# Kernel optimization log

Measured on AMD Instinct MI355X. Metric: run time of the kernel, lower is better.

The kernel has to match this reference:

```python
import jax, jax.numpy as jnp
import numpy as np

N_NODES = 100000
N_EDGES = 3200000
IN_CH = 128
HID = 128
N_CLASSES = 32
N_GRAPHS = 256


def gcn_conv(x, W, b, src, dst, n_nodes):
    """PyG GCNConv: add self-loops, symmetric deg^-1/2 normalization,
    linear transform, gather-scatter aggregation, bias."""
    xw = x @ W  # [N, out]
    loop = jnp.arange(n_nodes, dtype=src.dtype)
    s = jnp.concatenate([src, loop])  # sources incl. self-loops
    d = jnp.concatenate([dst, loop])  # targets incl. self-loops
    deg = jax.ops.segment_sum(jnp.ones_like(d, dtype=xw.dtype), d,
                              num_segments=n_nodes)
    dinv = jnp.where(deg > 0, jax.lax.rsqrt(deg), 0.0)
    norm = dinv[s] * dinv[d]  # [E+N]
    msgs = xw[s] * norm[:, None]  # gather + scale
    out = jax.ops.segment_sum(msgs, d, num_segments=n_nodes)  # scatter-add
    return out + b


def global_mean_pool(x, batch, n_graphs):
    sums = jax.ops.segment_sum(x, batch, num_segments=n_graphs)
    cnt = jax.ops.segment_sum(jnp.ones((x.shape[0],), x.dtype), batch,
                              num_segments=n_graphs)
    return sums / jnp.maximum(cnt, 1.0)[:, None]


def setup_inputs() -> dict:
    key = jax.random.key(0)
    ks = jax.random.split(key, 9)
    x = jax.random.normal(ks[0], (N_NODES, IN_CH), dtype=jnp.float32)
    edge_index = jax.random.randint(ks[1], (2, N_EDGES), 0, N_NODES, dtype=jnp.int32)
    batch = jnp.sort(jax.random.randint(ks[2], (N_NODES,), 0, N_GRAPHS, dtype=jnp.int32))
    s1 = 1.0 / np.sqrt(IN_CH)
    s2 = 1.0 / np.sqrt(HID)
    W1 = jax.random.uniform(ks[3], (IN_CH, HID), jnp.float32, -s1, s1)
    b1 = jnp.zeros((HID,), jnp.float32)
    W2 = jax.random.uniform(ks[4], (HID, HID), jnp.float32, -s2, s2)
    b2 = jnp.zeros((HID,), jnp.float32)
    Wfc = jax.random.uniform(ks[5], (HID, N_CLASSES), jnp.float32, -s2, s2)
    bfc = jax.random.uniform(ks[6], (N_CLASSES,), jnp.float32, -s2, s2)
    return {"x": x, "edge_index": edge_index, "batch": batch,
            "W1": W1, "b1": b1, "W2": W2, "b2": b2, "Wfc": Wfc, "bfc": bfc}


def reference(x, edge_index, batch, W1, b1, W2, b2, Wfc, bfc):
    src, dst = edge_index[0], edge_index[1]
    h = jax.nn.relu(gcn_conv(x, W1, b1, src, dst, N_NODES))
    h = jax.nn.relu(gcn_conv(h, W2, b2, src, dst, N_NODES))
    g = global_mean_pool(h, batch, N_GRAPHS)  # [G, HID]
    return g @ Wfc + bfc  # [G, N_CLASSES]
```

## Files before the change

### kernel.cpp

```cpp
#include <hip/hip_runtime.h>
#include <hip/hip_bf16.h>
#include <hip/hip_fp16.h>

static constexpr int CH     = 128;
static constexpr int NCLS   = 32;
static constexpr int NGRAPH = 256;

static constexpr int BSHIFT = 8;
static constexpr int BW     = 1 << BSHIFT;
static constexpr int MAXB   = 512;

typedef _Float16 half8 __attribute__((ext_vector_type(8)));
typedef _Float16 half4 __attribute__((ext_vector_type(4)));
typedef float    f32x4 __attribute__((ext_vector_type(4)));
typedef float    f32x2 __attribute__((ext_vector_type(2)));

static constexpr float FP8_SCALE = 64.0f;
static constexpr float FP8_INV   = 1.0f / 64.0f;

__device__ __forceinline__ f32x2 dec8(unsigned short u) {
  return __builtin_amdgcn_cvt_pk_f32_fp8((int)u, false);
}
__device__ __forceinline__ unsigned char enc8(float v) {
  return (unsigned char)(__builtin_amdgcn_cvt_pk_fp8_f32(v, v, 0, false) & 0xFF);
}

__global__ __launch_bounds__(256) void k_init_wt(
    int* __restrict__ gcur, int CAP, int NBUCK, int* __restrict__ xzero,
    const float* __restrict__ W1, const float* __restrict__ W2,
    _Float16* __restrict__ WhT1, _Float16* __restrict__ WhT2) {
  int t = threadIdx.x;
  if (blockIdx.x == 0) {
    for (int i = t; i < NBUCK; i += 256) gcur[i] = i * CAP;
    if (t < 32) xzero[t] = 0;
    return;
  }
  int i = (blockIdx.x - 1) * 256 + t;
  const float* W = (i < CH * CH) ? W1 : W2;
  _Float16* T   = (i < CH * CH) ? WhT1 : WhT2;
  int j = i & (CH * CH - 1);
  int k = j >> 7, n = j & 127;
  T[n * CH + k] = (_Float16)W[j];
}

__global__ __launch_bounds__(1024) void k_scatter(
    const int* __restrict__ src, const int* __restrict__ dst,
    int* __restrict__ gcur, int* __restrict__ ebuf, int E) {
  __shared__ int bcnt[MAXB];
  __shared__ int bbase[MAXB];
  int t = threadIdx.x;
  if (t < MAXB) bcnt[t] = 0;
  __syncthreads();
  int base = blockIdx.x * 8192;
  int s_[8], d_[8], r_[8];
  #pragma unroll
  for (int j = 0; j < 8; ++j) {
    int i = base + j * 1024 + t;
    if (i < E) {
      s_[j] = src[i];
      d_[j] = dst[i];
      r_[j] = atomicAdd(&bcnt[d_[j] >> BSHIFT], 1);
    }
  }
  __syncthreads();
  if (t < MAXB && bcnt[t]) bbase[t] = atomicAdd(&gcur[t], bcnt[t]);
  __syncthreads();
  #pragma unroll
  for (int j = 0; j < 8; ++j) {
    int i = base + j * 1024 + t;
    if (i < E) {
      int b = d_[j] >> BSHIFT;
      int p = ((d_[j] & (BW - 1)) << 17) | s_[j];
      ebuf[bbase[b] + r_[j]] = p;
    }
  }
}

__global__ __launch_bounds__(1024) void k_build(
    const int* __restrict__ ebuf, const int* __restrict__ gcur,
    int* __restrict__ offs, int* __restrict__ oend,
    float* __restrict__ dinv, int* __restrict__ csr, int N, int CAP) {
  __shared__ int sdeg[BW];
  __shared__ int sscan[BW];
  int b = blockIdx.x;
  int t = threadIdx.x;
  int lo = b << BSHIFT;
  int e0 = b * CAP;
  int e1 = gcur[b];

  if (t < BW) sdeg[t] = 0;
  __syncthreads();
  for (int e = e0 + t; e < e1; e += 1024)
    atomicAdd(&sdeg[ebuf[e] >> 17], 1);
  __syncthreads();
  if (t < BW) sscan[t] = (sdeg[t] + 3) & ~3;
  __syncthreads();
  for (int st = 1; st < BW; st <<= 1) {
    int v = (t < BW && t >= st) ? sscan[t - st] : 0;
    __syncthreads();
    if (t < BW) sscan[t] += v;
    __syncthreads();
  }
  if (t < BW) {
    int deg  = sdeg[t];
    int pdeg = (deg + 3) & ~3;
    int ex = b * CAP + sscan[t] - pdeg;
    int n = lo + t;
    if (n < N) {
      offs[n] = ex;
      oend[n] = ex + deg;
      dinv[n] = 1.0f / sqrtf((float)(deg + 1));
      for (int q = deg; q < pdeg; ++q) csr[ex + q] = N;
    }
    sscan[t] = ex;
  }
  __syncthreads();
  for (int e = e0 + t; e < e1; e += 1024) {
    int p = ebuf[e];
    int pos = atomicAdd(&sscan[p >> 17], 1);
    csr[pos] = p & 0x1FFFF;
  }
}

__device__ __forceinline__ void stage_w(const _Float16* __restrict__ WhT,
                                        _Float16 (*Ws)[136], int tid) {
  #pragma unroll
  for (int l = 0; l < 8; ++l) {
    int idx = tid + l * 256;
    int n = idx >> 4, k8 = (idx & 15) << 3;
    *(half8*)&Ws[n][k8] = *(const half8*)(WhT + n * CH + k8);
  }
}

__device__ __forceinline__ void gemm_core64(
    const _Float16 (*As)[136], const _Float16 (*Ws)[136],
    const float* __restrict__ dinv, unsigned char* __restrict__ C,
    int row0, int M, int tid) {
  int lane = tid & 63, wave = tid >> 6;
  int quad = lane >> 4, sub = lane & 15;
  int m0 = wave * 16;

  f32x4 acc[8];
  #pragma unroll
  for (int j = 0; j < 8; ++j) acc[j] = (f32x4){0.f, 0.f, 0.f, 0.f};

  #pragma unroll
  for (int kc = 0; kc < 4; ++kc) {
    int ko = kc * 32 + quad * 8;
    half8 a = *(const half8*)&As[m0 + sub][ko];
    #pragma unroll
    for (int nt = 0; nt < 8; ++nt) {
      half8 b = *(const half8*)&Ws[nt * 16 + sub][ko];
      acc[nt] = __builtin_amdgcn_mfma_f32_16x16x32_f16(a, b, acc[nt], 0, 0, 0);
    }
  }
  #pragma unroll
  for (int r = 0; r < 4; ++r) {
    int row = row0 + m0 + quad * 4 + r;
    if (row < M) {
      float d = dinv[row] * FP8_SCALE;
      #pragma unroll
      for (int nt = 0; nt < 8; ++nt)
        C[(size_t)row * CH + nt * 16 + sub] = enc8(acc[nt][r] * d);
    }
  }
}

__global__ __launch_bounds__(256) void k_gemm_f32(
    const float* __restrict__ A, const _Float16* __restrict__ WhT,
    const float* __restrict__ dinv, unsigned char* __restrict__ C, int M) {
  __shared__ _Float16 As[64][136];
  __shared__ _Float16 Ws[128][136];
  int tid = threadIdx.x;
  int row0 = blockIdx.x * 64;
  #pragma unroll
  for (int l = 0; l < 8; ++l) {
    int idx = tid + l * 256;
    int r = idx >> 5, c4 = (idx & 31) << 2;
    int rr = row0 + r; if (rr >= M) rr = M - 1;
    float4 v = *(const float4*)(A + (size_t)rr * CH + c4);
    half4 hv = { (_Float16)v.x, (_Float16)v.y, (_Float16)v.z, (_Float16)v.w };
    *(half4*)&As[r][c4] = hv;
  }
  stage_w(WhT, Ws, tid);
  __syncthreads();
  gemm_core64(As, Ws, dinv, C, row0, M, tid);
}

__global__ __launch_bounds__(256) void k_gemm_f16(
    const _Float16* __restrict__ A, const _Float16* __restrict__ WhT,
    const float* __restrict__ dinv, unsigned char* __restrict__ C, int M) {
  __shared__ _Float16 As[64][136];
  __shared__ _Float16 Ws[128][136];
  int tid = threadIdx.x;
  int row0 = blockIdx.x * 64;
  #pragma unroll
  for (int l = 0; l < 4; ++l) {
    int idx = tid + l * 256;
    int r = idx >> 4, c8 = (idx & 15) << 3;
    int rr = row0 + r; if (rr >= M) rr = M - 1;
    *(half8*)&As[r][c8] = *(const half8*)(A + (size_t)rr * CH + c8);
  }
  stage_w(WhT, Ws, tid);
  __syncthreads();
  gemm_core64(As, Ws, dinv, C, row0, M, tid);
}

__global__ __launch_bounds__(256) void k_agg(
    const unsigned char* __restrict__ xs, const int* __restrict__ csr,
    const int* __restrict__ offs, const int* __restrict__ oend,
    const float* __restrict__ dinv, const float* __restrict__ bias,
    __half* __restrict__ out, int N) {
  int wid  = blockIdx.x * 4 + (threadIdx.x >> 6);
  int lane = threadIdx.x & 63;
  int nA = wid * 2, nB = nA + 1;
  if (nA >= N) return;
  bool hasB = (nB < N);
  unsigned int lane2 = (unsigned int)lane << 1;

  int eA = offs[nA];
  int cA = (oend[nA] - eA + 3) >> 2;
  int eB = hasB ? offs[nB] : 0;
  int cB = hasB ? ((oend[nB] - eB + 3) >> 2) : 0;

  f32x2 aA0 = dec8(*(const unsigned short*)(xs + (((unsigned int)nA << 7) | lane2)));
  f32x2 aA1 = {0.f, 0.f};
  f32x2 aB0 = {0.f, 0.f}, aB1 = {0.f, 0.f};
  if (hasB)
    aB0 = dec8(*(const unsigned short*)(xs + (((unsigned int)nB << 7) | lane2)));

  while (cA > 0 && cB > 0) {
    int4 ca = *(const int4*)(csr + eA);
    int4 cb = *(const int4*)(csr + eB);
    unsigned short uA0 = *(const unsigned short*)(xs + (((unsigned int)ca.x << 7) | lane2));
    unsigned short uA1 = *(const unsigned short*)(xs + (((unsigned int)ca.y << 7) | lane2));
    unsigned short uA2 = *(const unsigned short*)(xs + (((unsigned int)ca.z << 7) | lane2));
    unsigned short uA3 = *(const unsigned short*)(xs + (((unsigned int)ca.w << 7) | lane2));
    unsigned short uB0 = *(const unsigned short*)(xs + (((unsigned int)cb.x << 7) | lane2));
    unsigned short uB1 = *(const unsigned short*)(xs + (((unsigned int)cb.y << 7) | lane2));
    unsigned short uB2 = *(const unsigned short*)(xs + (((unsigned int)cb.z << 7) | lane2));
    unsigned short uB3 = *(const unsigned short*)(xs + (((unsigned int)cb.w << 7) | lane2));
    aA0 += dec8(uA0); aA1 += dec8(uA1); aA0 += dec8(uA2); aA1 += dec8(uA3);
    aB0 += dec8(uB0); aB1 += dec8(uB1); aB0 += dec8(uB2); aB1 += dec8(uB3);
    eA += 4; eB += 4; --cA; --cB;
  }
  while (cA > 0) {
    int4 ca = *(const int4*)(csr + eA);
    unsigned short u0 = *(const unsigned short*)(xs + (((unsigned int)ca.x << 7) | lane2));
    unsigned short u1 = *(const unsigned short*)(xs + (((unsigned int)ca.y << 7) | lane2));
    unsigned short u2 = *(const unsigned short*)(xs + (((unsigned int)ca.z << 7) | lane2));
    unsigned short u3 = *(const unsigned short*)(xs + (((unsigned int)ca.w << 7) | lane2));
    aA0 += dec8(u0); aA1 += dec8(u1); aA0 += dec8(u2); aA1 += dec8(u3);
    eA += 4; --cA;
  }
  while (cB > 0) {
    int4 cb = *(const int4*)(csr + eB);
    unsigned short u0 = *(const unsigned short*)(xs + (((unsigned int)cb.x << 7) | lane2));
    unsigned short u1 = *(const unsigned short*)(xs + (((unsigned int)cb.y << 7) | lane2));
    unsigned short u2 = *(const unsigned short*)(xs + (((unsigned int)cb.z << 7) | lane2));
    unsigned short u3 = *(const unsigned short*)(xs + (((unsigned int)cb.w << 7) | lane2));
    aB0 += dec8(u0); aB1 += dec8(u1); aB0 += dec8(u2); aB1 += dec8(u3);
    eB += 4; --cB;
  }

  float2 bxy = *(const float2*)(bias + 2 * lane);
  {
    f32x2 s = aA0 + aA1;
    float dn = dinv[nA] * FP8_INV;
    float rx = fmaf(s[0], dn, bxy.x);
    float ry = fmaf(s[1], dn, bxy.y);
    ((__half2*)out)[(size_t)nA * 64 + lane] =
        __floats2half2_rn(fmaxf(rx, 0.f), fmaxf(ry, 0.f));
  }
  if (hasB) {
    f32x2 s = aB0 + aB1;
    float dn = dinv[nB] * FP8_INV;
    float rx = fmaf(s[0], dn, bxy.x);
    float ry = fmaf(s[1], dn, bxy.y);
    ((__half2*)out)[(size_t)nB * 64 + lane] =
        __floats2half2_rn(fmaxf(rx, 0.f), fmaxf(ry, 0.f));
  }
}

__global__ __launch_bounds__(128) void k_pool(
    const __half* __restrict__ h, const int* __restrict__ batch,
    float* __restrict__ gsum, int* __restrict__ gstart,
    int* __restrict__ gend, int N) {
  int ch = threadIdx.x;
  int n0 = blockIdx.x * 128;
  int n1 = n0 + 128; if (n1 > N) n1 = N;
  if (n0 >= N) return;
  for (int n = n0 + ch; n < n1; n += 128) {
    int g = batch[n];
    if (n == 0 || batch[n - 1] != g) gstart[g] = n;
    if (n == N - 1 || batch[n + 1] != g) gend[g] = n + 1;
  }
  float acc = 0.f;
  int curg = batch[n0];
  for (int n = n0; n < n1; ++n) {
    int g = batch[n];
    if (g != curg) {
      atomicAdd(&gsum[curg * CH + ch], acc);
      acc = 0.f; curg = g;
    }
    acc += __half2float(h[(size_t)n * CH + ch]);
  }
  atomicAdd(&gsum[curg * CH + ch], acc);
}

__global__ __launch_bounds__(64) void k_fc(
    const float* __restrict__ gsum, const int* __restrict__ gstart,
    const int* __restrict__ gend, const float* __restrict__ Wfc,
    const float* __restrict__ bfc, float* __restrict__ outp) {
  int g = blockIdx.x;
  int j = threadIdx.x;
  if (j >= NCLS) return;
  int cnt = gend[g] - gstart[g];
  float invc = 1.0f / fmaxf((float)cnt, 1.0f);
  float acc = 0.0f;
  for (int c = 0; c < CH; ++c)
    acc = fmaf(gsum[g * CH + c], Wfc[c * NCLS + j], acc);
  outp[g * NCLS + j] = fmaf(acc, invc, bfc[j]);
}

extern "C" void kernel_launch(void* const* d_in, const int* in_sizes, int n_in,
                              void* d_out, int out_size, void* d_ws, size_t ws_size,
                              hipStream_t stream) {
  const float* x    = (const float*)d_in[0];
  const int*   ei   = (const int*)d_in[1];
  const int*   batch= (const int*)d_in[2];
  const float* W1   = (const float*)d_in[3];
  const float* b1   = (const float*)d_in[4];
  const float* W2   = (const float*)d_in[5];
  const float* b2   = (const float*)d_in[6];
  const float* Wfc  = (const float*)d_in[7];
  const float* bfc  = (const float*)d_in[8];
  float* outp = (float*)d_out;

  const int N = in_sizes[0] / CH;
  const int E = in_sizes[1] / 2;
  const int* src = ei;
  const int* dst = ei + E;
  const int NBUCK = (N + BW - 1) >> BSHIFT;
  int CAP = (E / NBUCK) + (E / NBUCK) / 8 + 1280;
  CAP = (CAP + 3) & ~3;

  char* w = (char*)d_ws;
  size_t o = 0;
  auto carve = [&](size_t bytes) -> void* {
    o = (o + 255) & ~(size_t)255;
    void* p = w + o;
    o += bytes;
    return p;
  };
  float*    gsum   = (float*)   carve((size_t)NGRAPH * CH * 4);
  int*      gstart = (int*)     carve((size_t)NGRAPH * 4);
  int*      gend   = (int*)     carve((size_t)NGRAPH * 4);
  size_t zbytes = o;
  int*      offs   = (int*)     carve((size_t)N * 4);
  int*      oendb  = (int*)     carve((size_t)N * 4);
  int*      gcur   = (int*)     carve(MAXB * 4);
  int*      csr    = (int*)     carve((size_t)NBUCK * CAP * 4);
  float*    dinv   = (float*)   carve((size_t)N * 4);
  _Float16* WhT1   = (_Float16*)carve((size_t)CH * CH * 2);
  _Float16* WhT2   = (_Float16*)carve((size_t)CH * CH * 2);
  unsigned char* xsbuf = (unsigned char*)carve((size_t)(N + 1) * CH);
  __half*   hbuf   = (__half*)  carve((size_t)N * CH * 2);
  (void)ws_size;

  int* ebuf = (int*)hbuf;

  (void)hipMemsetAsync(gsum, 0, zbytes, stream);

  const int GB64 = (N + 63) / 64;
  const int GB   = (N + 127) / 128;
  const int AB   = (N + 7) / 8;

  k_init_wt<<<129, 256, 0, stream>>>(gcur, CAP, NBUCK,
                                     (int*)(xsbuf + (size_t)N * CH),
                                     W1, W2, WhT1, WhT2);
  k_scatter<<<(E + 8191) / 8192, 1024, 0, stream>>>(src, dst, gcur, ebuf, E);
  k_build  <<<NBUCK, 1024, 0, stream>>>(ebuf, gcur, offs, oendb, dinv, csr, N, CAP);

  k_gemm_f32<<<GB64, 256, 0, stream>>>(x, WhT1, dinv, xsbuf, N);
  k_agg<<<AB, 256, 0, stream>>>(xsbuf, csr, offs, oendb, dinv, b1, hbuf, N);
  k_gemm_f16<<<GB64, 256, 0, stream>>>((const _Float16*)hbuf, WhT2, dinv, xsbuf, N);
  k_agg<<<AB, 256, 0, stream>>>(xsbuf, csr, offs, oendb, dinv, b2, hbuf, N);

  k_pool<<<GB, 128, 0, stream>>>(hbuf, batch, gsum, gstart, gend, N);
  k_fc<<<NGRAPH, 64, 0, stream>>>(gsum, gstart, gend, Wfc, bfc, outp);
  (void)out_size; (void)n_in;
}
```

Before: 360.5 us.

## Use persistent grid-stride aggregation with 8-wide unrolled gathers and prefetched indices

The aggregation kernel becomes a persistent grid-stride loop capped at 2048 blocks, where each wave processes node pairs repeatedly instead of launching one wave per pair. The inner loop now issues 16 gathers per iteration, 8 edges per node, and prefetches the next CSR index quads while the current gathers are in flight, to raise memory-level parallelism. Tails are drained in 8- and 4-edge chunks. The cost is higher register pressure and possible load imbalance across the fixed grid. It also reads CSR entries one iteration ahead, which depends on padding after each segment.

```diff
diff --git a/kernel.cpp b/kernel.cpp
--- a/kernel.cpp
+++ b/kernel.cpp
@@ -211,74 +211,88 @@
     const int* __restrict__ offs, const int* __restrict__ oend,
     const float* __restrict__ dinv, const float* __restrict__ bias,
     __half* __restrict__ out, int N) {
-  int wid  = blockIdx.x * 4 + (threadIdx.x >> 6);
-  int lane = threadIdx.x & 63;
-  int nA = wid * 2, nB = nA + 1;
-  if (nA >= N) return;
-  bool hasB = (nB < N);
+  int wid0  = blockIdx.x * 4 + (threadIdx.x >> 6);
+  int lane  = threadIdx.x & 63;
+  int wstep = gridDim.x * 4;
   unsigned int lane2 = (unsigned int)lane << 1;
-
-  int eA = offs[nA];
-  int cA = (oend[nA] - eA + 3) >> 2;
-  int eB = hasB ? offs[nB] : 0;
-  int cB = hasB ? ((oend[nB] - eB + 3) >> 2) : 0;
-
-  f32x2 aA0 = dec8(*(const unsigned short*)(xs + (((unsigned int)nA << 7) | lane2)));
-  f32x2 aA1 = {0.f, 0.f};
-  f32x2 aB0 = {0.f, 0.f}, aB1 = {0.f, 0.f};
-  if (hasB)
-    aB0 = dec8(*(const unsigned short*)(xs + (((unsigned int)nB << 7) | lane2)));
-
-  while (cA > 0 && cB > 0) {
-    int4 ca = *(const int4*)(csr + eA);
-    int4 cb = *(const int4*)(csr + eB);
-    unsigned short uA0 = *(const unsigned short*)(xs + (((unsigned int)ca.x << 7) | lane2));
-    unsigned short uA1 = *(const unsigned short*)(xs + (((unsigned int)ca.y << 7) | lane2));
-    unsigned short uA2 = *(const unsigned short*)(xs + (((unsigned int)ca.z << 7) | lane2));
-    unsigned short uA3 = *(const unsigned short*)(xs + (((unsigned int)ca.w << 7) | lane2));
-    unsigned short uB0 = *(const unsigned short*)(xs + (((unsigned int)cb.x << 7) | lane2));
-    unsigned short uB1 = *(const unsigned short*)(xs + (((unsigned int)cb.y << 7) | lane2));
-    unsigned short uB2 = *(const unsigned short*)(xs + (((unsigned int)cb.z << 7) | lane2));
-    unsigned short uB3 = *(const unsigned short*)(xs + (((unsigned int)cb.w << 7) | lane2));
-    aA0 += dec8(uA0); aA1 += dec8(uA1); aA0 += dec8(uA2); aA1 += dec8(uA3);
-    aB0 += dec8(uB0); aB1 += dec8(uB1); aB0 += dec8(uB2); aB1 += dec8(uB3);
-    eA += 4; eB += 4; --cA; --cB;
-  }
-  while (cA > 0) {
-    int4 ca = *(const int4*)(csr + eA);
-    unsigned short u0 = *(const unsigned short*)(xs + (((unsigned int)ca.x << 7) | lane2));
-    unsigned short u1 = *(const unsigned short*)(xs + (((unsigned int)ca.y << 7) | lane2));
-    unsigned short u2 = *(const unsigned short*)(xs + (((unsigned int)ca.z << 7) | lane2));
-    unsigned short u3 = *(const unsigned short*)(xs + (((unsigned int)ca.w << 7) | lane2));
-    aA0 += dec8(u0); aA1 += dec8(u1); aA0 += dec8(u2); aA1 += dec8(u3);
-    eA += 4; --cA;
-  }
-  while (cB > 0) {
-    int4 cb = *(const int4*)(csr + eB);
-    unsigned short u0 = *(const unsigned short*)(xs + (((unsigned int)cb.x << 7) | lane2));
-    unsigned short u1 = *(const unsigned short*)(xs + (((unsigned int)cb.y << 7) | lane2));
-    unsigned short u2 = *(const unsigned short*)(xs + (((unsigned int)cb.z << 7) | lane2));
-    unsigned short u3 = *(const unsigned short*)(xs + (((unsigned int)cb.w << 7) | lane2));
-    aB0 += dec8(u0); aB1 += dec8(u1); aB0 += dec8(u2); aB1 += dec8(u3);
-    eB += 4; --cB;
-  }
-
   float2 bxy = *(const float2*)(bias + 2 * lane);
-  {
-    f32x2 s = aA0 + aA1;
-    float dn = dinv[nA] * FP8_INV;
-    float rx = fmaf(s[0], dn, bxy.x);
-    float ry = fmaf(s[1], dn, bxy.y);
-    ((__half2*)out)[(size_t)nA * 64 + lane] =
-        __floats2half2_rn(fmaxf(rx, 0.f), fmaxf(ry, 0.f));
-  }
-  if (hasB) {
-    f32x2 s = aB0 + aB1;
-    float dn = dinv[nB] * FP8_INV;
-    float rx = fmaf(s[0], dn, bxy.x);
-    float ry = fmaf(s[1], dn, bxy.y);
-    ((__half2*)out)[(size_t)nB * 64 + lane] =
-        __floats2half2_rn(fmaxf(rx, 0.f), fmaxf(ry, 0.f));
+
+  auto g = [&](int s) -> unsigned short {
+    return *(const unsigned short*)(xs + (((unsigned int)s << 7) | lane2));
+  };
+
+  for (int wid = wid0; wid * 2 < N; wid += wstep) {
+    int nA = wid * 2, nB = nA + 1;
+    bool hasB = (nB < N);
+
+    int eA = offs[nA];
+    int cA = (oend[nA] - eA + 3) >> 2;
+    int eB = hasB ? offs[nB] : eA;
+    int cB = hasB ? ((oend[nB] - eB + 3) >> 2) : 0;
+
+    f32x2 aA0 = dec8(g(nA));
+    f32x2 aA1 = {0.f, 0.f};
+    f32x2 aB0 = {0.f, 0.f}, aB1 = {0.f, 0.f};
+    if (hasB) aB0 = dec8(g(nB));
+
+    if (cA >= 2 && cB >= 2) {
+      int4 ca0 = *(const int4*)(csr + eA);
+      int4 ca1 = *(const int4*)(csr + eA + 4);
+      int4 cb0 = *(const int4*)(csr + eB);
+      int4 cb1 = *(const int4*)(csr + eB + 4);
+      do {
+        unsigned short uA0 = g(ca0.x), uA1 = g(ca0.y), uA2 = g(ca0.z), uA3 = g(ca0.w);
+        unsigned short uA4 = g(ca1.x), uA5 = g(ca1.y), uA6 = g(ca1.z), uA7 = g(ca1.w);
+        unsigned short uB0 = g(cb0.x), uB1 = g(cb0.y), uB2 = g(cb0.z), uB3 = g(cb0.w);
+        unsigned short uB4 = g(cb1.x), uB5 = g(cb1.y), uB6 = g(cb1.z), uB7 = g(cb1.w);
+        eA += 8; eB += 8; cA -= 2; cB -= 2;
+        int4 na0 = *(const int4*)(csr + eA);
+        int4 na1 = *(const int4*)(csr + eA + 4);
+        int4 nb0 = *(const int4*)(csr + eB);
+        int4 nb1 = *(const int4*)(csr + eB + 4);
+        aA0 += dec8(uA0); aA1 += dec8(uA1); aA0 += dec8(uA2); aA1 += dec8(uA3);
+        aA0 += dec8(uA4); aA1 += dec8(uA5); aA0 += dec8(uA6); aA1 += dec8(uA7);
+        aB0 += dec8(uB0); aB1 += dec8(uB1); aB0 += dec8(uB2); aB1 += dec8(uB3);
+        aB0 += dec8(uB4); aB1 += dec8(uB5); aB0 += dec8(uB6); aB1 += dec8(uB7);
+        ca0 = na0; ca1 = na1; cb0 = nb0; cb1 = nb1;
+      } while (cA >= 2 && cB >= 2);
+    }
+
+    auto drain = [&](int e, int c, f32x2& a0, f32x2& a1) {
+      while (c >= 2) {
+        int4 q0 = *(const int4*)(csr + e);
+        int4 q1 = *(const int4*)(csr + e + 4);
+        unsigned short u0 = g(q0.x), u1 = g(q0.y), u2 = g(q0.z), u3 = g(q0.w);
+        unsigned short u4 = g(q1.x), u5 = g(q1.y), u6 = g(q1.z), u7 = g(q1.w);
+        a0 += dec8(u0); a1 += dec8(u1); a0 += dec8(u2); a1 += dec8(u3);
+        a0 += dec8(u4); a1 += dec8(u5); a0 += dec8(u6); a1 += dec8(u7);
+        e += 8; c -= 2;
+      }
+      if (c > 0) {
+        int4 q0 = *(const int4*)(csr + e);
+        unsigned short u0 = g(q0.x), u1 = g(q0.y), u2 = g(q0.z), u3 = g(q0.w);
+        a0 += dec8(u0); a1 += dec8(u1); a0 += dec8(u2); a1 += dec8(u3);
+      }
+    };
+    drain(eA, cA, aA0, aA1);
+    if (hasB) drain(eB, cB, aB0, aB1);
+
+    {
+      f32x2 s = aA0 + aA1;
+      float dn = dinv[nA] * FP8_INV;
+      float rx = fmaf(s[0], dn, bxy.x);
+      float ry = fmaf(s[1], dn, bxy.y);
+      ((__half2*)out)[(size_t)nA * 64 + lane] =
+          __floats2half2_rn(fmaxf(rx, 0.f), fmaxf(ry, 0.f));
+    }
+    if (hasB) {
+      f32x2 s = aB0 + aB1;
+      float dn = dinv[nB] * FP8_INV;
+      float rx = fmaf(s[0], dn, bxy.x);
+      float ry = fmaf(s[1], dn, bxy.y);
+      ((__half2*)out)[(size_t)nB * 64 + lane] =
+          __floats2half2_rn(fmaxf(rx, 0.f), fmaxf(ry, 0.f));
+    }
   }
 }
 
@@ -374,7 +388,8 @@
 
   const int GB64 = (N + 63) / 64;
   const int GB   = (N + 127) / 128;
-  const int AB   = (N + 7) / 8;
+  int AB = (N + 7) / 8;
+  if (AB > 2048) AB = 2048;
 
   k_init_wt<<<129, 256, 0, stream>>>(gcur, CAP, NBUCK,
                                      (int*)(xsbuf + (size_t)N * CH),
```

Result: faster. 350.0 us (-2.9%).

## Restructure aggregation to 8 edges per wave with 16-byte row gathers

Applied to the files above, without the earlier changes.

The aggregation kernel now handles one node per wave with a grid-stride loop. Eight lanes split each 128-byte fp8 row into 16-byte chunks, so a wave gathers eight neighbour rows at once, and the partial sums are combined with cross-lane shuffles. The CSR build pads each node's list to a multiple of eight and inserts the self-loop as an explicit entry. This replaces the old 2-byte-per-lane gathers with wide loads and larger in-flight parallelism, at the cost of more padding entries, shuffle reductions and a larger per-bucket capacity.

```diff
diff --git a/kernel.cpp b/kernel.cpp
--- a/kernel.cpp
+++ b/kernel.cpp
@@ -18,9 +18,6 @@
 static constexpr float FP8_SCALE = 64.0f;
 static constexpr float FP8_INV   = 1.0f / 64.0f;
 
-__device__ __forceinline__ f32x2 dec8(unsigned short u) {
-  return __builtin_amdgcn_cvt_pk_f32_fp8((int)u, false);
-}
 __device__ __forceinline__ unsigned char enc8(float v) {
   return (unsigned char)(__builtin_amdgcn_cvt_pk_fp8_f32(v, v, 0, false) & 0xFF);
 }
@@ -93,7 +90,7 @@
   for (int e = e0 + t; e < e1; e += 1024)
     atomicAdd(&sdeg[ebuf[e] >> 17], 1);
   __syncthreads();
-  if (t < BW) sscan[t] = (sdeg[t] + 3) & ~3;
+  if (t < BW) sscan[t] = (sdeg[t] + 8) & ~7;
   __syncthreads();
   for (int st = 1; st < BW; st <<= 1) {
     int v = (t < BW && t >= st) ? sscan[t - st] : 0;
@@ -103,14 +100,15 @@
   }
   if (t < BW) {
     int deg  = sdeg[t];
-    int pdeg = (deg + 3) & ~3;
+    int pdeg = (deg + 8) & ~7;
     int ex = b * CAP + sscan[t] - pdeg;
     int n = lo + t;
     if (n < N) {
       offs[n] = ex;
-      oend[n] = ex + deg;
+      oend[n] = ex + pdeg;
       dinv[n] = 1.0f / sqrtf((float)(deg + 1));
-      for (int q = deg; q < pdeg; ++q) csr[ex + q] = N;
+      csr[ex + deg] = n;
+      for (int q = deg + 1; q < pdeg; ++q) csr[ex + q] = N;
     }
     sscan[t] = ex;
   }
@@ -207,78 +205,83 @@
 }
 
 __global__ __launch_bounds__(256) void k_agg(
-    const unsigned char* __restrict__ xs, const int* __restrict__ csr,
+    const uint4* __restrict__ xs4, const int* __restrict__ csr,
     const int* __restrict__ offs, const int* __restrict__ oend,
     const float* __restrict__ dinv, const float* __restrict__ bias,
     __half* __restrict__ out, int N) {
-  int wid  = blockIdx.x * 4 + (threadIdx.x >> 6);
-  int lane = threadIdx.x & 63;
-  int nA = wid * 2, nB = nA + 1;
-  if (nA >= N) return;
-  bool hasB = (nB < N);
-  unsigned int lane2 = (unsigned int)lane << 1;
-
-  int eA = offs[nA];
-  int cA = (oend[nA] - eA + 3) >> 2;
-  int eB = hasB ? offs[nB] : 0;
-  int cB = hasB ? ((oend[nB] - eB + 3) >> 2) : 0;
-
-  f32x2 aA0 = dec8(*(const unsigned short*)(xs + (((unsigned int)nA << 7) | lane2)));
-  f32x2 aA1 = {0.f, 0.f};
-  f32x2 aB0 = {0.f, 0.f}, aB1 = {0.f, 0.f};
-  if (hasB)
-    aB0 = dec8(*(const unsigned short*)(xs + (((unsigned int)nB << 7) | lane2)));
-
-  while (cA > 0 && cB > 0) {
-    int4 ca = *(const int4*)(csr + eA);
-    int4 cb = *(const int4*)(csr + eB);
-    unsigned short uA0 = *(const unsigned short*)(xs + (((unsigned int)ca.x << 7) | lane2));
-    unsigned short uA1 = *(const unsigned short*)(xs + (((unsigned int)ca.y << 7) | lane2));
-    unsigned short uA2 = *(const unsigned short*)(xs + (((unsigned int)ca.z << 7) | lane2));
-    unsigned short uA3 = *(const unsigned short*)(xs + (((unsigned int)ca.w << 7) | lane2));
-    unsigned short uB0 = *(const unsigned short*)(xs + (((unsigned int)cb.x << 7) | lane2));
-    unsigned short uB1 = *(const unsigned short*)(xs + (((unsigned int)cb.y << 7) | lane2));
-    unsigned short uB2 = *(const unsigned short*)(xs + (((unsigned int)cb.z << 7) | lane2));
-    unsigned short uB3 = *(const unsigned short*)(xs + (((unsigned int)cb.w << 7) | lane2));
-    aA0 += dec8(uA0); aA1 += dec8(uA1); aA0 += dec8(uA2); aA1 += dec8(uA3);
-    aB0 += dec8(uB0); aB1 += dec8(uB1); aB0 += dec8(uB2); aB1 += dec8(uB3);
-    eA += 4; eB += 4; --cA; --cB;
-  }
-  while (cA > 0) {
-    int4 ca = *(const int4*)(csr + eA);
-    unsigned short u0 = *(const unsigned short*)(xs + (((unsigned int)ca.x << 7) | lane2));
-    unsigned short u1 = *(const unsigned short*)(xs + (((unsigned int)ca.y << 7) | lane2));
-    unsigned short u2 = *(const unsigned short*)(xs + (((unsigned int)ca.z << 7) | lane2));
-    unsigned short u3 = *(const unsigned short*)(xs + (((unsigned int)ca.w << 7) | lane2));
-    aA0 += dec8(u0); aA1 += dec8(u1); aA0 += dec8(u2); aA1 += dec8(u3);
-    eA += 4; --cA;
-  }
-  while (cB > 0) {
-    int4 cb = *(const int4*)(csr + eB);
-    unsigned short u0 = *(const unsigned short*)(xs + (((unsigned int)cb.x << 7) | lane2));
-    unsigned short u1 = *(const unsigned short*)(xs + (((unsigned int)cb.y << 7) | lane2));
-    unsigned short u2 = *(const unsigned short*)(xs + (((unsigned int)cb.z << 7) | lane2));
-    unsigned short u3 = *(const unsigned short*)(xs + (((unsigned int)cb.w << 7) | lane2));
-    aB0 += dec8(u0); aB1 += dec8(u1); aB0 += dec8(u2); aB1 += dec8(u3);
-    eB += 4; --cB;
-  }
-
-  float2 bxy = *(const float2*)(bias + 2 * lane);
-  {
-    f32x2 s = aA0 + aA1;
-    float dn = dinv[nA] * FP8_INV;
-    float rx = fmaf(s[0], dn, bxy.x);
-    float ry = fmaf(s[1], dn, bxy.y);
-    ((__half2*)out)[(size_t)nA * 64 + lane] =
-        __floats2half2_rn(fmaxf(rx, 0.f), fmaxf(ry, 0.f));
-  }
-  if (hasB) {
-    f32x2 s = aB0 + aB1;
-    float dn = dinv[nB] * FP8_INV;
-    float rx = fmaf(s[0], dn, bxy.x);
-    float ry = fmaf(s[1], dn, bxy.y);
-    ((__half2*)out)[(size_t)nB * 64 + lane] =
-        __floats2half2_rn(fmaxf(rx, 0.f), fmaxf(ry, 0.f));
+  int lane  = threadIdx.x & 63;
+  int w0    = blockIdx.x * 4 + (threadIdx.x >> 6);
+  int wstep = gridDim.x * 4;
+  int e = lane >> 3, c = lane & 7;
+
+  float4 bb0 = *(const float4*)(bias + c * 16);
+  float4 bb1 = *(const float4*)(bias + c * 16 + 4);
+  float4 bb2 = *(const float4*)(bias + c * 16 + 8);
+  float4 bb3 = *(const float4*)(bias + c * 16 + 12);
+
+  for (int n = w0; n < N; n += wstep) {
+    int base = offs[n];
+    int ng = (oend[n] - base) >> 3;
+
+    f32x2 a[8];
+    #pragma unroll
+    for (int j = 0; j < 8; ++j) a[j] = (f32x2){0.f, 0.f};
+
+    auto acc8 = [&](uint4 q) {
+      a[0] += __builtin_amdgcn_cvt_pk_f32_fp8((int)q.x, false);
+      a[1] += __builtin_amdgcn_cvt_pk_f32_fp8((int)q.x, true);
+      a[2] += __builtin_amdgcn_cvt_pk_f32_fp8((int)q.y, false);
+      a[3] += __builtin_amdgcn_cvt_pk_f32_fp8((int)q.y, true);
+      a[4] += __builtin_amdgcn_cvt_pk_f32_fp8((int)q.z, false);
+      a[5] += __builtin_amdgcn_cvt_pk_f32_fp8((int)q.z, true);
+      a[6] += __builtin_amdgcn_cvt_pk_f32_fp8((int)q.w, false);
+      a[7] += __builtin_amdgcn_cvt_pk_f32_fp8((int)q.w, true);
+    };
+
+    int p = base + e;
+    int g = 0;
+    for (; g + 2 <= ng; g += 2, p += 16) {
+      int s0 = csr[p];
+      int s1 = csr[p + 8];
+      uint4 q0 = xs4[((unsigned int)s0 << 3) | (unsigned int)c];
+      uint4 q1 = xs4[((unsigned int)s1 << 3) | (unsigned int)c];
+      acc8(q0);
+      acc8(q1);
+    }
+    if (g < ng) {
+      int s0 = csr[p];
+      uint4 q0 = xs4[((unsigned int)s0 << 3) | (unsigned int)c];
+      acc8(q0);
+    }
+
+    #pragma unroll
+    for (int m = 8; m <= 32; m <<= 1) {
+      #pragma unroll
+      for (int j = 0; j < 8; ++j) {
+        f32x2 t;
+        t[0] = __shfl_xor(a[j][0], m);
+        t[1] = __shfl_xor(a[j][1], m);
+        a[j] += t;
+      }
+    }
+
+    if (e == 0) {
+      float dn = dinv[n] * FP8_INV;
+      float bf[16] = {bb0.x, bb0.y, bb0.z, bb0.w,
+                      bb1.x, bb1.y, bb1.z, bb1.w,
+                      bb2.x, bb2.y, bb2.z, bb2.w,
+                      bb3.x, bb3.y, bb3.z, bb3.w};
+      __half2 hh[8];
+      #pragma unroll
+      for (int j = 0; j < 8; ++j) {
+        float rx = fmaf(a[j][0], dn, bf[2 * j]);
+        float ry = fmaf(a[j][1], dn, bf[2 * j + 1]);
+        hh[j] = __floats2half2_rn(fmaxf(rx, 0.f), fmaxf(ry, 0.f));
+      }
+      __half* orow = out + (size_t)n * CH + c * 16;
+      *(uint4*)orow = *(uint4*)&hh[0];
+      *(uint4*)(orow + 8) = *(uint4*)&hh[4];
+    }
   }
 }
 
@@ -342,8 +345,8 @@
   const int* src = ei;
   const int* dst = ei + E;
   const int NBUCK = (N + BW - 1) >> BSHIFT;
-  int CAP = (E / NBUCK) + (E / NBUCK) / 8 + 1280;
-  CAP = (CAP + 3) & ~3;
+  int CAP = (E / NBUCK) + (E / NBUCK) / 8 + 2048 + 256;
+  CAP = (CAP + 7) & ~7;
 
   char* w = (char*)d_ws;
   size_t o = 0;
@@ -374,7 +377,8 @@
 
   const int GB64 = (N + 63) / 64;
   const int GB   = (N + 127) / 128;
-  const int AB   = (N + 7) / 8;
+  int AB = (N + 3) / 4;
+  if (AB > 2048) AB = 2048;
 
   k_init_wt<<<129, 256, 0, stream>>>(gcur, CAP, NBUCK,
                                      (int*)(xsbuf + (size_t)N * CH),
@@ -383,9 +387,9 @@
   k_build  <<<NBUCK, 1024, 0, stream>>>(ebuf, gcur, offs, oendb, dinv, csr, N, CAP);
 
   k_gemm_f32<<<GB64, 256, 0, stream>>>(x, WhT1, dinv, xsbuf, N);
-  k_agg<<<AB, 256, 0, stream>>>(xsbuf, csr, offs, oendb, dinv, b1, hbuf, N);
+  k_agg<<<AB, 256, 0, stream>>>((const uint4*)xsbuf, csr, offs, oendb, dinv, b1, hbuf, N);
   k_gemm_f16<<<GB64, 256, 0, stream>>>((const _Float16*)hbuf, WhT2, dinv, xsbuf, N);
-  k_agg<<<AB, 256, 0, stream>>>(xsbuf, csr, offs, oendb, dinv, b2, hbuf, N);
+  k_agg<<<AB, 256, 0, stream>>>((const uint4*)xsbuf, csr, offs, oendb, dinv, b2, hbuf, N);
 
   k_pool<<<GB, 128, 0, stream>>>(hbuf, batch, gsum, gstart, gend, N);
   k_fc<<<NGRAPH, 64, 0, stream>>>(gsum, gstart, gend, Wfc, bfc, outp);
```

New measurement: 395.0 us. 1.1x slower.
